# Kernel optimization log

Measured on AMD Instinct MI355X. Metric: run time of the kernel, lower is better.

## Reference

```python
import jax, jax.numpy as jnp
import numpy as np

B, T, H, W, C = 2, 8, 64, 64, 256
HEADS = 8
WS = 8


def setup_inputs() -> dict:
    key = jax.random.key(0)
    k1, k2, k3 = jax.random.split(key, 3)
    x = jax.random.normal(k1, (B, T, H, W, C), dtype=jnp.float32)
    qkv_w = jax.random.normal(k2, (C, 3 * C), dtype=jnp.float32) * (C ** -0.5)
    proj_w = jax.random.normal(k3, (C, C), dtype=jnp.float32) * (C ** -0.5)
    proj_b = jnp.zeros((C,), dtype=jnp.float32)
    return {"x": x, "qkv_w": qkv_w, "proj_w": proj_w, "proj_b": proj_b}


def reference(x, qkv_w, proj_w, proj_b):
    b, t, h, w, c = x.shape
    hn, wn = h // WS, w // WS
    dh = c // HEADS
    scale = dh ** -0.5
    # window partition: (B,T,H,W,C) -> (B*hn*wn, T*WS*WS, C)
    xw = x.reshape(b, t, hn, WS, wn, WS, c)
    xw = jnp.transpose(xw, (0, 2, 4, 1, 3, 5, 6)).reshape(-1, t * WS * WS, c)
    bw, n, _ = xw.shape
    qkv = (xw @ qkv_w).reshape(bw, n, 3, HEADS, dh)
    qkv = jnp.transpose(qkv, (2, 0, 3, 1, 4))  # (3, Bw, heads, N, dh)
    q, k, v = qkv[0], qkv[1], qkv[2]
    attn = jax.nn.softmax(jnp.einsum("bhnd,bhmd->bhnm", q, k) * scale, axis=-1)
    out = jnp.einsum("bhnm,bhmd->bhnd", attn, v)
    out = jnp.transpose(out, (0, 2, 1, 3)).reshape(bw, n, c)
    out = out @ proj_w + proj_b
    # window reverse
    out = out.reshape(b, hn, wn, t, WS, WS, c)
    out = jnp.transpose(out, (0, 3, 1, 4, 2, 5, 6)).reshape(b, t, h, w, c)
    return out
```

## Files before the change

### kernel.cpp

```cpp
#include <hip/hip_runtime.h>


typedef __bf16 bf16x8 __attribute__((ext_vector_type(8)));
typedef float f32x4 __attribute__((ext_vector_type(4)));
typedef float f32x16 __attribute__((ext_vector_type(16)));

#define NTOK 512
#define DH 32
#define CDIM 256
#define C3 768

__device__ __forceinline__ unsigned short f2b(float f) {
  unsigned u = __builtin_bit_cast(unsigned, f);
  unsigned r = u + 0x7fffu + ((u >> 16) & 1u);
  return (unsigned short)(r >> 16);
}

__device__ __forceinline__ unsigned pk2(float a, float b) {
  __bf16 x = (__bf16)a, y = (__bf16)b;
  return (unsigned)__builtin_bit_cast(unsigned short, x) |
         ((unsigned)__builtin_bit_cast(unsigned short, y) << 16);
}

__global__ void k_prep(const float* __restrict__ qkv_w, const float* __restrict__ proj_w,
                       unsigned short* __restrict__ wqT, unsigned short* __restrict__ wpT) {
  const float QS = 0.2550540254f;
  int idx = blockIdx.x * 256 + threadIdx.x;
  int stride = gridDim.x * 256;
  for (int i = idx; i < C3 * CDIM; i += stride) {
    int n = i >> 8, kk = i & 255;
    float f = qkv_w[kk * C3 + n];
    if (n < 256) f *= QS;
    wqT[i] = f2b(f);
  }
  for (int i = idx; i < CDIM * CDIM; i += stride) {
    int n = i >> 8, kk = i & 255;
    wpT[i] = f2b(proj_w[kk * CDIM + n]);
  }
}

__global__ __launch_bounds__(256, 2) void k_qkv(
    const float* __restrict__ x, const unsigned short* __restrict__ wqT,
    unsigned short* __restrict__ qo, unsigned short* __restrict__ ko,
    unsigned short* __restrict__ vo) {
  extern __shared__ char smem[];
  unsigned short (*As)[264] = (unsigned short (*)[264])smem;
  unsigned short (*Bs)[40]  = (unsigned short (*)[40])(smem + 128 * 264 * 2);
  int tid = threadIdx.x;
  int mtile = blockIdx.x;
  int bw = mtile >> 2;
  int n0 = (mtile & 3) << 7;
  int bb = bw >> 6, hi = (bw >> 3) & 7, wi = bw & 7;

  {
    int row = tid >> 1;
    int n = n0 + row;
    int tt = n >> 6, ii = (n >> 3) & 7, jj = n & 7;
    const float* src = x + ((((long)(bb * 8 + tt)) * 64 + (hi * 8 + ii)) * 64 + (wi * 8 + jj)) * 256;
    int fb = (tid & 1) * 4;
#pragma unroll
    for (int u = 0; u < 32; ++u) {
      int f = fb + u * 8;
      float4 d = *(const float4*)(src + f);
      __bf16 h0 = (__bf16)d.x, h1 = (__bf16)d.y, h2 = (__bf16)d.z, h3 = (__bf16)d.w;
      __bf16* dst = (__bf16*)&As[row][f];
      dst[0] = h0; dst[1] = h1; dst[2] = h2; dst[3] = h3;
    }
  }
  __syncthreads();

  int wid = tid >> 6, lane = tid & 63;
  int lg = lane >> 4, lr = lane & 15;
  int wr = wid >> 1, wc = wid & 1;

  for (int nt = 0; nt < 6; ++nt) {
    f32x4 acc[4][4];
#pragma unroll
    for (int a = 0; a < 4; ++a)
#pragma unroll
      for (int b2 = 0; b2 < 4; ++b2) acc[a][b2] = (f32x4){0.f, 0.f, 0.f, 0.f};

    for (int kk = 0; kk < 256; kk += 32) {
      __syncthreads();
      {
        int brow = tid >> 1, bh2 = tid & 1;
        const uint4* bs = (const uint4*)(wqT + ((long)(nt * 128 + brow)) * 256 + kk + bh2 * 16);
        uint4 b0 = bs[0], b1 = bs[1];
        *(uint4*)&Bs[brow][bh2 * 16] = b0;
        *(uint4*)&Bs[brow][bh2 * 16 + 8] = b1;
      }
      __syncthreads();
      bf16x8 af[4], bfr[4];
#pragma unroll
      for (int mi = 0; mi < 4; ++mi)
        af[mi] = *(const bf16x8*)&As[wr * 64 + mi * 16 + lr][kk + lg * 8];
#pragma unroll
      for (int ni = 0; ni < 4; ++ni)
        bfr[ni] = *(const bf16x8*)&Bs[wc * 64 + ni * 16 + lr][lg * 8];
#pragma unroll
      for (int mi = 0; mi < 4; ++mi)
#pragma unroll
        for (int ni = 0; ni < 4; ++ni)
          acc[mi][ni] = __builtin_amdgcn_mfma_f32_16x16x32_bf16(af[mi], bfr[ni], acc[mi][ni], 0, 0, 0);
    }
#pragma unroll
    for (int ni = 0; ni < 4; ++ni) {
      int c = nt * 128 + wc * 64 + ni * 16 + lr;
      int which = c >> 8, d = c & 31;
      long base = ((long)(bw * 8 + ((c >> 5) & 7))) * 16384;
      if (which == 2) {
#pragma unroll
        for (int mi = 0; mi < 4; ++mi) {
          int m = n0 + wr * 64 + mi * 16 + lg * 4;
          long off = base + ((long)((m >> 5) * 4 + ((m >> 4) & 1) * 2 + ((m >> 3) & 1)) * 32 + d) * 8 + (m & 7);
          ushort4 w;
          __bf16 v0 = (__bf16)acc[mi][ni][0], v1 = (__bf16)acc[mi][ni][1];
          __bf16 v2 = (__bf16)acc[mi][ni][2], v3 = (__bf16)acc[mi][ni][3];
          w.x = __builtin_bit_cast(unsigned short, v0);
          w.y = __builtin_bit_cast(unsigned short, v1);
          w.z = __builtin_bit_cast(unsigned short, v2);
          w.w = __builtin_bit_cast(unsigned short, v3);
          *(ushort4*)&vo[off] = w;
        }
      } else {
        unsigned short* dst = (which == 0) ? qo : ko;
        int cb = (d >> 4) * 2 + ((d >> 3) & 1);
        int dj = d & 7;
#pragma unroll
        for (int mi = 0; mi < 4; ++mi) {
#pragma unroll
          for (int r = 0; r < 4; ++r) {
            int n = n0 + wr * 64 + mi * 16 + lg * 4 + r;
            long off = base + ((long)((n >> 5) * 4 + cb) * 32 + (n & 31)) * 8 + dj;
            __bf16 hv = (__bf16)acc[mi][ni][r];
            dst[off] = __builtin_bit_cast(unsigned short, hv);
          }
        }
      }
    }
  }
}

__global__ __launch_bounds__(256, 2) void k_attn(
    const unsigned short* __restrict__ qs0, const unsigned short* __restrict__ ks0,
    const unsigned short* __restrict__ vs0, unsigned short* __restrict__ og) {
  extern __shared__ char smem[];
  int bh = blockIdx.x, tid = threadIdx.x;
  const unsigned short* kg = ks0 + (long)bh * 16384;
  const unsigned short* vg = vs0 + (long)bh * 16384;
#pragma unroll
  for (int i = 0; i < 8; ++i) {
    int ci = tid + i * 256;
    *(uint4*)(smem + ci * 16) = *(const uint4*)(kg + ci * 8);
    *(uint4*)(smem + 32768 + ci * 16) = *(const uint4*)(vg + ci * 8);
  }
  __syncthreads();

  int wid = tid >> 6, lane = tid & 63;
  int l31 = lane & 31, h = lane >> 5;
  const unsigned short* qb = qs0 + (long)bh * 16384;
  unsigned short* ob = og + (long)bh * 16384;
  const f32x16 z16 = {0.f,0.f,0.f,0.f,0.f,0.f,0.f,0.f,0.f,0.f,0.f,0.f,0.f,0.f,0.f,0.f};

  bf16x8 qf[4][2];
#pragma unroll
  for (int qt = 0; qt < 4; ++qt)
#pragma unroll
    for (int ks = 0; ks < 2; ++ks)
      qf[qt][ks] = *(const bf16x8*)(qb + ((wid * 4 + qt) * 4 + ks * 2 + h) * 256 + l31 * 8);

  f32x16 o[4];
  float ps[4];
#pragma unroll
  for (int qt = 0; qt < 4; ++qt) { o[qt] = z16; ps[qt] = 0.f; }

  for (int mt = 0; mt < 16; ++mt) {
    bf16x8 k0 = *(const bf16x8*)(smem + (mt * 4 + h) * 512 + l31 * 16);
    bf16x8 k1 = *(const bf16x8*)(smem + (mt * 4 + 2 + h) * 512 + l31 * 16);
    bf16x8 v0 = *(const bf16x8*)(smem + 32768 + (mt * 4 + h) * 512 + l31 * 16);
    bf16x8 v1 = *(const bf16x8*)(smem + 32768 + (mt * 4 + 2 + h) * 512 + l31 * 16);
#pragma unroll
    for (int qt = 0; qt < 4; ++qt) {
      f32x16 s = __builtin_amdgcn_mfma_f32_32x32x16_bf16(k0, qf[qt][0], z16, 0, 0, 0);
      s = __builtin_amdgcn_mfma_f32_32x32x16_bf16(k1, qf[qt][1], s, 0, 0, 0);
      float p[16];
#pragma unroll
      for (int r = 0; r < 16; ++r) p[r] = __builtin_amdgcn_exp2f(s[r]);
      ps[qt] += ((((p[0] + p[1]) + (p[2] + p[3])) + ((p[4] + p[5]) + (p[6] + p[7]))) +
                 (((p[8] + p[9]) + (p[10] + p[11])) + ((p[12] + p[13]) + (p[14] + p[15]))));
      unsigned w0 = pk2(p[0], p[1]),  w1 = pk2(p[2], p[3]);
      unsigned w2 = pk2(p[4], p[5]),  w3 = pk2(p[6], p[7]);
      unsigned w4 = pk2(p[8], p[9]),  w5 = pk2(p[10], p[11]);
      unsigned w6 = pk2(p[12], p[13]), w7 = pk2(p[14], p[15]);
      asm("v_permlane32_swap_b32 %0, %1" : "+v"(w0), "+v"(w2));
      asm("v_permlane32_swap_b32 %0, %1" : "+v"(w1), "+v"(w3));
      asm("v_permlane32_swap_b32 %0, %1" : "+v"(w4), "+v"(w6));
      asm("v_permlane32_swap_b32 %0, %1" : "+v"(w5), "+v"(w7));
      uint4 pb0u; pb0u.x = w0; pb0u.y = w1; pb0u.z = w2; pb0u.w = w3;
      uint4 pb1u; pb1u.x = w4; pb1u.y = w5; pb1u.z = w6; pb1u.w = w7;
      bf16x8 pb0 = __builtin_bit_cast(bf16x8, pb0u);
      bf16x8 pb1 = __builtin_bit_cast(bf16x8, pb1u);
      o[qt] = __builtin_amdgcn_mfma_f32_32x32x16_bf16(v0, pb0, o[qt], 0, 0, 0);
      o[qt] = __builtin_amdgcn_mfma_f32_32x32x16_bf16(v1, pb1, o[qt], 0, 0, 0);
    }
  }

#pragma unroll
  for (int qt = 0; qt < 4; ++qt) {
    float sum = ps[qt] + __shfl_xor(ps[qt], 32, 64);
    float rcp = 1.0f / sum;
    int q = (wid * 4 + qt) * 32 + l31;
#pragma unroll
    for (int s4 = 0; s4 < 4; ++s4) {
      __bf16 b0 = (__bf16)(o[qt][s4 * 4 + 0] * rcp);
      __bf16 b1 = (__bf16)(o[qt][s4 * 4 + 1] * rcp);
      __bf16 b2 = (__bf16)(o[qt][s4 * 4 + 2] * rcp);
      __bf16 b3 = (__bf16)(o[qt][s4 * 4 + 3] * rcp);
      ushort4 w;
      w.x = __builtin_bit_cast(unsigned short, b0);
      w.y = __builtin_bit_cast(unsigned short, b1);
      w.z = __builtin_bit_cast(unsigned short, b2);
      w.w = __builtin_bit_cast(unsigned short, b3);
      *(ushort4*)(ob + q * 32 + s4 * 8 + h * 4) = w;
    }
  }
}

__global__ __launch_bounds__(256, 2) void k_proj(
    const unsigned short* __restrict__ og, const unsigned short* __restrict__ wpT,
    const float* __restrict__ pb, float* __restrict__ out) {
  extern __shared__ char smem[];
  unsigned short (*As)[264] = (unsigned short (*)[264])smem;
  unsigned short (*Bs)[40]  = (unsigned short (*)[40])(smem + 128 * 264 * 2);
  int tid = threadIdx.x;
  int mtile = blockIdx.x;
  int bw = mtile >> 2;
  int n0 = (mtile & 3) << 7;
  int bb = bw >> 6, hi = (bw >> 3) & 7, wi = bw & 7;

  {
    int row = tid >> 1, hf = tid & 1;
#pragma unroll
    for (int h4 = 0; h4 < 4; ++h4) {
      int h = hf * 4 + h4;
      const uint4* asrc = (const uint4*)(og + (((long)(bw * 8 + h)) * NTOK + n0 + row) * DH);
      uint4 d0 = asrc[0], d1 = asrc[1], d2 = asrc[2], d3 = asrc[3];
      *(uint4*)&As[row][h * 32]      = d0;
      *(uint4*)&As[row][h * 32 + 8]  = d1;
      *(uint4*)&As[row][h * 32 + 16] = d2;
      *(uint4*)&As[row][h * 32 + 24] = d3;
    }
  }
  __syncthreads();

  int wid = tid >> 6, lane = tid & 63;
  int lg = lane >> 4, lr = lane & 15;
  int wr = wid >> 1, wc = wid & 1;

  for (int nt = 0; nt < 2; ++nt) {
    f32x4 acc[4][4];
#pragma unroll
    for (int a = 0; a < 4; ++a)
#pragma unroll
      for (int b2 = 0; b2 < 4; ++b2) acc[a][b2] = (f32x4){0.f, 0.f, 0.f, 0.f};

    for (int kk = 0; kk < 256; kk += 32) {
      __syncthreads();
      {
        int brow = tid >> 1, bh2 = tid & 1;
        const uint4* bs = (const uint4*)(wpT + ((long)(nt * 128 + brow)) * 256 + kk + bh2 * 16);
        uint4 b0 = bs[0], b1 = bs[1];
        *(uint4*)&Bs[brow][bh2 * 16] = b0;
        *(uint4*)&Bs[brow][bh2 * 16 + 8] = b1;
      }
      __syncthreads();
      bf16x8 af[4], bfr[4];
#pragma unroll
      for (int mi = 0; mi < 4; ++mi)
        af[mi] = *(const bf16x8*)&As[wr * 64 + mi * 16 + lr][kk + lg * 8];
#pragma unroll
      for (int ni = 0; ni < 4; ++ni)
        bfr[ni] = *(const bf16x8*)&Bs[wc * 64 + ni * 16 + lr][lg * 8];
#pragma unroll
      for (int mi = 0; mi < 4; ++mi)
#pragma unroll
        for (int ni = 0; ni < 4; ++ni)
          acc[mi][ni] = __builtin_amdgcn_mfma_f32_16x16x32_bf16(af[mi], bfr[ni], acc[mi][ni], 0, 0, 0);
    }
#pragma unroll
    for (int ni = 0; ni < 4; ++ni) {
      int c = nt * 128 + wc * 64 + ni * 16 + lr;
      float bias = pb[c];
#pragma unroll
      for (int mi = 0; mi < 4; ++mi) {
        int nbase = n0 + wr * 64 + mi * 16 + lg * 4;
#pragma unroll
        for (int r = 0; r < 4; ++r) {
          int n = nbase + r;
          int tt = n >> 6, ii = (n >> 3) & 7, jj = n & 7;
          long off = ((((long)(bb * 8 + tt)) * 64 + (hi * 8 + ii)) * 64 + (wi * 8 + jj)) * 256 + c;
          out[off] = acc[mi][ni][r] + bias;
        }
      }
    }
  }
}

extern "C" void kernel_launch(void* const* d_in, const int* in_sizes, int n_in,
                              void* d_out, int out_size, void* d_ws, size_t ws_size,
                              hipStream_t stream) {
  const float* x      = (const float*)d_in[0];
  const float* qkv_w  = (const float*)d_in[1];
  const float* proj_w = (const float*)d_in[2];
  const float* proj_b = (const float*)d_in[3];
  float* out = (float*)d_out;
  char* ws = (char*)d_ws;

  unsigned short* wqT = (unsigned short*)(ws);
  unsigned short* wpT = (unsigned short*)(ws + 393216);
  unsigned short* Q   = (unsigned short*)(ws + 524288);
  unsigned short* K   = (unsigned short*)(ws + 524288 + 1L * 33554432);
  unsigned short* V   = (unsigned short*)(ws + 524288 + 2L * 33554432);
  unsigned short* O   = (unsigned short*)(ws + 524288 + 3L * 33554432);

  (void)hipFuncSetAttribute((const void*)k_qkv,  hipFuncAttributeMaxDynamicSharedMemorySize, 77824);
  (void)hipFuncSetAttribute((const void*)k_attn, hipFuncAttributeMaxDynamicSharedMemorySize, 65536);
  (void)hipFuncSetAttribute((const void*)k_proj, hipFuncAttributeMaxDynamicSharedMemorySize, 77824);

  k_prep<<<256, 256, 0, stream>>>(qkv_w, proj_w, wqT, wpT);
  k_qkv<<<512, 256, 77824, stream>>>(x, wqT, Q, K, V);
  k_attn<<<1024, 256, 65536, stream>>>(Q, K, V, O);
  k_proj<<<512, 256, 77824, stream>>>(O, wpT, proj_b, out);
}
```

Measured before the change: 144.4 us.

## Load weight fragments directly from global and vectorize Q/K stores via LDS transpose

Both GEMM kernels stop staging weight tiles through shared memory and the two __syncthreads per k-step; each warp loads its MFMA B fragments directly from global memory, relying on L2/L1 caching of the small weight matrices. The Q/K output path in k_qkv now writes each 16-row accumulator slab into a small per-warp shared buffer and reads it back as 16-byte rows, replacing scattered 2-byte global stores with wide stores. This trades barrier overhead and poor store coalescing for more global load traffic on weights and extra LDS traffic in the epilogue.

```diff
diff --git a/kernel.cpp b/kernel.cpp
--- a/kernel.cpp
+++ b/kernel.cpp
@@ -45,7 +45,6 @@
     unsigned short* __restrict__ vo) {
   extern __shared__ char smem[];
   unsigned short (*As)[264] = (unsigned short (*)[264])smem;
-  unsigned short (*Bs)[40]  = (unsigned short (*)[40])(smem + 128 * 264 * 2);
   int tid = threadIdx.x;
   int mtile = blockIdx.x;
   int bw = mtile >> 2;
@@ -72,6 +71,7 @@
   int wid = tid >> 6, lane = tid & 63;
   int lg = lane >> 4, lr = lane & 15;
   int wr = wid >> 1, wc = wid & 1;
+  unsigned short* Ts = (unsigned short*)(smem + 67584) + wid * 16 * 88;
 
   for (int nt = 0; nt < 6; ++nt) {
     f32x4 acc[4][4];
@@ -80,35 +80,50 @@
 #pragma unroll
       for (int b2 = 0; b2 < 4; ++b2) acc[a][b2] = (f32x4){0.f, 0.f, 0.f, 0.f};
 
+    const unsigned short* bb2 = wqT + ((long)(nt * 128 + wc * 64)) * 256;
     for (int kk = 0; kk < 256; kk += 32) {
-      __syncthreads();
-      {
-        int brow = tid >> 1, bh2 = tid & 1;
-        const uint4* bs = (const uint4*)(wqT + ((long)(nt * 128 + brow)) * 256 + kk + bh2 * 16);
-        uint4 b0 = bs[0], b1 = bs[1];
-        *(uint4*)&Bs[brow][bh2 * 16] = b0;
-        *(uint4*)&Bs[brow][bh2 * 16 + 8] = b1;
-      }
-      __syncthreads();
       bf16x8 af[4], bfr[4];
+#pragma unroll
+      for (int ni = 0; ni < 4; ++ni)
+        bfr[ni] = *(const bf16x8*)(bb2 + (ni * 16 + lr) * 256 + kk + lg * 8);
 #pragma unroll
       for (int mi = 0; mi < 4; ++mi)
         af[mi] = *(const bf16x8*)&As[wr * 64 + mi * 16 + lr][kk + lg * 8];
 #pragma unroll
-      for (int ni = 0; ni < 4; ++ni)
-        bfr[ni] = *(const bf16x8*)&Bs[wc * 64 + ni * 16 + lr][lg * 8];
-#pragma unroll
       for (int mi = 0; mi < 4; ++mi)
 #pragma unroll
         for (int ni = 0; ni < 4; ++ni)
           acc[mi][ni] = __builtin_amdgcn_mfma_f32_16x16x32_bf16(af[mi], bfr[ni], acc[mi][ni], 0, 0, 0);
     }
-#pragma unroll
-    for (int ni = 0; ni < 4; ++ni) {
-      int c = nt * 128 + wc * 64 + ni * 16 + lr;
-      int which = c >> 8, d = c & 31;
-      long base = ((long)(bw * 8 + ((c >> 5) & 7))) * 16384;
-      if (which == 2) {
+
+    if (nt < 4) {
+      unsigned short* dst = (nt < 2) ? qo : ko;
+      int head0 = (nt * 4 + wc * 2) & 7;
+      long base0 = ((long)(bw * 8 + head0)) * 16384;
+      long base1 = ((long)(bw * 8 + head0 + 1)) * 16384;
+      int row = lane >> 2, c2 = lane & 3;
+#pragma unroll
+      for (int mi = 0; mi < 4; ++mi) {
+#pragma unroll
+        for (int ni = 0; ni < 4; ++ni)
+#pragma unroll
+          for (int r = 0; r < 4; ++r) {
+            __bf16 hv = (__bf16)acc[mi][ni][r];
+            Ts[(lg * 4 + r) * 88 + ni * 16 + lr] = __builtin_bit_cast(unsigned short, hv);
+          }
+        int n = n0 + wr * 64 + mi * 16 + row;
+        long toff = ((long)((n >> 5) * 4 + c2)) * 256 + (n & 31) * 8;
+        uint4 d0 = *(const uint4*)&Ts[row * 88 + c2 * 8];
+        *(uint4*)&dst[base0 + toff] = d0;
+        uint4 d1 = *(const uint4*)&Ts[row * 88 + 32 + c2 * 8];
+        *(uint4*)&dst[base1 + toff] = d1;
+      }
+    } else {
+#pragma unroll
+      for (int ni = 0; ni < 4; ++ni) {
+        int c = nt * 128 + wc * 64 + ni * 16 + lr;
+        int d = c & 31;
+        long base = ((long)(bw * 8 + ((c >> 5) & 7))) * 16384;
 #pragma unroll
         for (int mi = 0; mi < 4; ++mi) {
           int m = n0 + wr * 64 + mi * 16 + lg * 4;
@@ -121,20 +136,6 @@
           w.z = __builtin_bit_cast(unsigned short, v2);
           w.w = __builtin_bit_cast(unsigned short, v3);
           *(ushort4*)&vo[off] = w;
-        }
-      } else {
-        unsigned short* dst = (which == 0) ? qo : ko;
-        int cb = (d >> 4) * 2 + ((d >> 3) & 1);
-        int dj = d & 7;
-#pragma unroll
-        for (int mi = 0; mi < 4; ++mi) {
-#pragma unroll
-          for (int r = 0; r < 4; ++r) {
-            int n = n0 + wr * 64 + mi * 16 + lg * 4 + r;
-            long off = base + ((long)((n >> 5) * 4 + cb) * 32 + (n & 31)) * 8 + dj;
-            __bf16 hv = (__bf16)acc[mi][ni][r];
-            dst[off] = __builtin_bit_cast(unsigned short, hv);
-          }
         }
       }
     }
@@ -231,7 +232,6 @@
     const float* __restrict__ pb, float* __restrict__ out) {
   extern __shared__ char smem[];
   unsigned short (*As)[264] = (unsigned short (*)[264])smem;
-  unsigned short (*Bs)[40]  = (unsigned short (*)[40])(smem + 128 * 264 * 2);
   int tid = threadIdx.x;
   int mtile = blockIdx.x;
   int bw = mtile >> 2;
@@ -264,23 +264,15 @@
 #pragma unroll
       for (int b2 = 0; b2 < 4; ++b2) acc[a][b2] = (f32x4){0.f, 0.f, 0.f, 0.f};
 
+    const unsigned short* bb2 = wpT + ((long)(nt * 128 + wc * 64)) * 256;
     for (int kk = 0; kk < 256; kk += 32) {
-      __syncthreads();
-      {
-        int brow = tid >> 1, bh2 = tid & 1;
-        const uint4* bs = (const uint4*)(wpT + ((long)(nt * 128 + brow)) * 256 + kk + bh2 * 16);
-        uint4 b0 = bs[0], b1 = bs[1];
-        *(uint4*)&Bs[brow][bh2 * 16] = b0;
-        *(uint4*)&Bs[brow][bh2 * 16 + 8] = b1;
-      }
-      __syncthreads();
       bf16x8 af[4], bfr[4];
+#pragma unroll
+      for (int ni = 0; ni < 4; ++ni)
+        bfr[ni] = *(const bf16x8*)(bb2 + (ni * 16 + lr) * 256 + kk + lg * 8);
 #pragma unroll
       for (int mi = 0; mi < 4; ++mi)
         af[mi] = *(const bf16x8*)&As[wr * 64 + mi * 16 + lr][kk + lg * 8];
-#pragma unroll
-      for (int ni = 0; ni < 4; ++ni)
-        bfr[ni] = *(const bf16x8*)&Bs[wc * 64 + ni * 16 + lr][lg * 8];
 #pragma unroll
       for (int mi = 0; mi < 4; ++mi)
 #pragma unroll
@@ -323,12 +315,12 @@
   unsigned short* V   = (unsigned short*)(ws + 524288 + 2L * 33554432);
   unsigned short* O   = (unsigned short*)(ws + 524288 + 3L * 33554432);
 
-  (void)hipFuncSetAttribute((const void*)k_qkv,  hipFuncAttributeMaxDynamicSharedMemorySize, 77824);
+  (void)hipFuncSetAttribute((const void*)k_qkv,  hipFuncAttributeMaxDynamicSharedMemorySize, 78848);
   (void)hipFuncSetAttribute((const void*)k_attn, hipFuncAttributeMaxDynamicSharedMemorySize, 65536);
-  (void)hipFuncSetAttribute((const void*)k_proj, hipFuncAttributeMaxDynamicSharedMemorySize, 77824);
+  (void)hipFuncSetAttribute((const void*)k_proj, hipFuncAttributeMaxDynamicSharedMemorySize, 67584);
 
   k_prep<<<256, 256, 0, stream>>>(qkv_w, proj_w, wqT, wpT);
-  k_qkv<<<512, 256, 77824, stream>>>(x, wqT, Q, K, V);
+  k_qkv<<<512, 256, 78848, stream>>>(x, wqT, Q, K, V);
   k_attn<<<1024, 256, 65536, stream>>>(Q, K, V, O);
-  k_proj<<<512, 256, 77824, stream>>>(O, wpT, proj_b, out);
-}
+  k_proj<<<512, 256, 67584, stream>>>(O, wpT, proj_b, out);
+}
```

Result: slower. 156.2 us (+8.2%).
